# Kernel tuning notes

Hardware: AMD Instinct MI355X
Metric: run time of the kernel (lower is better)

The kernel has to match this reference:

```python
import jax, jax.numpy as jnp
import numpy as np
import math

D_MODEL = 1024
NUM_HEADS = 16
HEAD_DIM = D_MODEL // NUM_HEADS
BATCH = 2
SEQ = 2048
THETA = 10000.0


def _rope_tables(seq_len, head_dim, theta=THETA):
    inv_freq = 1.0 / theta ** (jnp.arange(0, head_dim, 2, dtype=jnp.float32) / head_dim)
    pos = jnp.arange(seq_len, dtype=jnp.float32)
    freqs = jnp.outer(pos, inv_freq)                 # [S, hd/2]
    emb = jnp.concatenate([freqs, freqs], axis=-1)   # [S, hd]
    return jnp.cos(emb), jnp.sin(emb)


def _rotate_half(x):
    x1, x2 = jnp.split(x, 2, axis=-1)
    return jnp.concatenate([-x2, x1], axis=-1)


def setup_inputs() -> dict:
    key = jax.random.key(0)
    k1, k2, k3 = jax.random.split(key, 3)
    x = jax.random.normal(k1, (BATCH, SEQ, D_MODEL), dtype=jnp.float32)
    # causal mask: 1 where attend allowed, 0 where masked
    mask = jnp.tril(jnp.ones((SEQ, SEQ), dtype=jnp.int32))[None, None]
    w_qkv = jax.random.normal(k2, (D_MODEL, 3 * D_MODEL), dtype=jnp.float32) / math.sqrt(D_MODEL)
    w_out = jax.random.normal(k3, (D_MODEL, D_MODEL), dtype=jnp.float32) / math.sqrt(D_MODEL)
    return {"x": x, "mask": mask, "w_qkv": w_qkv, "w_out": w_out}


def reference(x, mask, w_qkv, w_out):
    B, S, _ = x.shape
    qkv = x @ w_qkv                                          # [B,S,3*D]
    qkv = qkv.reshape(B, S, 3, NUM_HEADS, HEAD_DIM)
    qkv = jnp.transpose(qkv, (2, 0, 3, 1, 4))                # [3,B,H,S,hd]
    q, k, v = qkv[0], qkv[1], qkv[2]
    cos, sin = _rope_tables(S, HEAD_DIM)                     # [S,hd]
    cos = cos[None, None]; sin = sin[None, None]
    q = q * cos + _rotate_half(q) * sin
    k = k * cos + _rotate_half(k) * sin
    scores = jnp.einsum('bhqd,bhkd->bhqk', q, k) / math.sqrt(HEAD_DIM)
    scores = jnp.where(mask == 0, -jnp.inf, scores)
    attn = jax.nn.softmax(scores, axis=-1)                   # dropout p=0 (eval)
    out = jnp.einsum('bhqk,bhkd->bhqd', attn, v)             # [B,H,S,hd]
    out = jnp.transpose(out, (0, 2, 1, 3)).reshape(B, S, D_MODEL)
    return out @ w_out
```

## Files before the change

### kernel.cpp

```cpp
#include <hip/hip_runtime.h>

typedef __bf16 bf16;
typedef __bf16 bf16x4 __attribute__((ext_vector_type(4)));
typedef __bf16 bf16x8 __attribute__((ext_vector_type(8)));
typedef short s16x4 __attribute__((ext_vector_type(4)));
typedef float f32x4 __attribute__((ext_vector_type(4)));

constexpr int BATCH = 2;
constexpr int SEQ   = 2048;
constexpr int DMODEL= 1024;
constexpr int NH    = 16;
constexpr int HD    = 64;
constexpr int M_ROWS= BATCH * SEQ;
constexpr int N_QKV = 3 * DMODEL;

__device__ __forceinline__ void gl_lds16(const bf16* g, bf16* l) {
  __builtin_amdgcn_global_load_lds(
      (const __attribute__((address_space(1))) unsigned int*)g,
      (__attribute__((address_space(3))) unsigned int*)l, 16, 0, 0);
}

__device__ __forceinline__ f32x4 mfma_16x16x16_bf16(bf16x4 a, bf16x4 b,
                                                    f32x4 c) {
#if defined(__HIP_DEVICE_COMPILE__)
  union { bf16x4 h; s16x4 s; } ua{a}, ub{b};
  return __builtin_amdgcn_mfma_f32_16x16x16bf16_1k(ua.s, ub.s, c, 0, 0, 0);
#else
  return c;
#endif
}

__global__ __launch_bounds__(256) void transpose_cast_kernel(
    const float* __restrict__ src, bf16* __restrict__ dst, int R, int C) {
  __shared__ float tile[32][33];
  const int c0 = blockIdx.x * 32, r0 = blockIdx.y * 32;
  const int tx = threadIdx.x, ty = threadIdx.y;
#pragma unroll
  for (int i = 0; i < 4; i++)
    tile[ty + 8 * i][tx] = src[(size_t)(r0 + ty + 8 * i) * C + c0 + tx];
  __syncthreads();
#pragma unroll
  for (int i = 0; i < 4; i++)
    dst[(size_t)(c0 + ty + 8 * i) * R + r0 + tx] = (bf16)tile[tx][ty + 8 * i];
}

__global__ __launch_bounds__(256) void cast_f32_bf16(
    const float* __restrict__ src, bf16* __restrict__ dst) {
  const int i = (blockIdx.x * 256 + threadIdx.x) * 8;
  float4 f0 = *(const float4*)&src[i];
  float4 f1 = *(const float4*)&src[i + 4];
  bf16x8 v;
  v[0] = (bf16)f0.x; v[1] = (bf16)f0.y; v[2] = (bf16)f0.z; v[3] = (bf16)f0.w;
  v[4] = (bf16)f1.x; v[5] = (bf16)f1.y; v[6] = (bf16)f1.z; v[7] = (bf16)f1.w;
  *(bf16x8*)&dst[i] = v;
}

#define GEMM_BODY(A, BT, K)                                                    \
  __shared__ bf16 As[128 * 32];                                                \
  __shared__ bf16 Bs[128 * 32];                                                \
  const int t = threadIdx.x;                                                   \
  const int m0 = blockIdx.y * 128;                                             \
  const int n0 = blockIdx.x * 128;                                             \
  const int w = t >> 6, lane = t & 63, g = lane >> 4, li = lane & 15;          \
  const int r0w = (w & 1) * 64, c0w = (w >> 1) * 64;                           \
  f32x4 acc[4][4] = {};                                                        \
  for (int k0 = 0; k0 < (K); k0 += 32) {                                       \
    __syncthreads();                                                           \
    _Pragma("unroll") for (int c = 0; c < 2; c++) {                            \
      const int idx = (w * 2 + c) * 64 + lane;                                 \
      const int row = idx >> 2, col = (idx & 3) * 8;                           \
      gl_lds16(&(A)[(size_t)(m0 + row) * (K) + k0 + col],                      \
               &As[(w * 2 + c) * 512]);                                        \
      gl_lds16(&(BT)[(size_t)(n0 + row) * (K) + k0 + col],                     \
               &Bs[(w * 2 + c) * 512]);                                        \
    }                                                                          \
    __syncthreads();                                                           \
    bf16x8 a[4], b[4];                                                         \
    _Pragma("unroll") for (int mt = 0; mt < 4; mt++)                           \
        a[mt] = *(const bf16x8*)&As[(r0w + mt * 16 + li) * 32 + g * 8];        \
    _Pragma("unroll") for (int nt = 0; nt < 4; nt++)                           \
        b[nt] = *(const bf16x8*)&Bs[(c0w + nt * 16 + li) * 32 + g * 8];        \
    _Pragma("unroll") for (int mt = 0; mt < 4; mt++)                           \
        _Pragma("unroll") for (int nt = 0; nt < 4; nt++)                       \
            acc[mt][nt] = __builtin_amdgcn_mfma_f32_16x16x32_bf16(             \
                a[mt], b[nt], acc[mt][nt], 0, 0, 0);                           \
  }

__global__ __launch_bounds__(256) void gemm_out(
    const bf16* __restrict__ A, const bf16* __restrict__ BT,
    float* __restrict__ C, int M, int N, int K) {
  GEMM_BODY(A, BT, K)
#pragma unroll
  for (int mt = 0; mt < 4; mt++)
#pragma unroll
    for (int nt = 0; nt < 4; nt++)
#pragma unroll
      for (int r = 0; r < 4; r++) {
        const int m = m0 + r0w + mt * 16 + g * 4 + r;
        const int n = n0 + c0w + nt * 16 + li;
        C[(size_t)m * N + n] = acc[mt][nt][r];
      }
}

__global__ __launch_bounds__(256) void gemm_qkv_rope(
    const bf16* __restrict__ A, const bf16* __restrict__ BT,
    bf16* __restrict__ Qb, bf16* __restrict__ Kb, bf16* __restrict__ Vt) {
  constexpr int K = DMODEL;
  GEMM_BODY(A, BT, K)

  const int region = n0 >> 10;
  const int b = m0 >> 11;
  const int h = ((n0 + c0w) >> 6) & 15;
  const size_t bh = (size_t)(b * NH + h);

  if (region < 2) {
    bf16* dst = region == 0 ? Qb : Kb;
    const float outsc = region == 0 ? 0.125f * 1.44269504f : 1.f;
    const float L = 13.287712379549449f;
    const float if0 = exp2f(-(float)(2 * li) / 64.f * L);
    const float if1 = exp2f(-(float)(2 * (li + 16)) / 64.f * L);
#pragma unroll
    for (int mt = 0; mt < 4; mt++)
#pragma unroll
      for (int r = 0; r < 4; r++) {
        const int s = (m0 + r0w + mt * 16 + g * 4 + r) & (SEQ - 1);
        float cs[2], sn[2];
        __sincosf((float)s * if0, &sn[0], &cs[0]);
        __sincosf((float)s * if1, &sn[1], &cs[1]);
#pragma unroll
        for (int nt = 0; nt < 4; nt++) {
          const int d = nt * 16 + li;
          const int par = nt & 1;
          const float a = acc[mt][nt][r];
          const float ap = acc[mt][nt ^ 2][r];
          const float v = (nt < 2) ? a * cs[par] - ap * sn[par]
                                   : a * cs[par] + ap * sn[par];
          dst[(bh * SEQ + s) * HD + d] = (bf16)(v * outsc);
        }
      }
  } else {
#pragma unroll
    for (int mt = 0; mt < 4; mt++)
#pragma unroll
      for (int nt = 0; nt < 4; nt++) {
        const int s = (m0 + r0w + mt * 16 + g * 4) & (SEQ - 1);
        const int d = nt * 16 + li;
        bf16x4 v;
#pragma unroll
        for (int r = 0; r < 4; r++) v[r] = (bf16)acc[mt][nt][r];
        *(bf16x4*)&Vt[(bh * HD + d) * SEQ + s] = v;
      }
  }
}

__global__ __launch_bounds__(512, 4) void flash_attn6(
    const bf16* __restrict__ Q, const bf16* __restrict__ Kb,
    const bf16* __restrict__ Vt, bf16* __restrict__ Oout) {
  const int f = blockIdx.x;
  const int c = f & 255, half = f >> 8;
  const int bh = c >> 3, idx = c & 7;
  const int qt = half ? 15 - idx : idx;
  const int q0 = qt * 128;
  const int t = threadIdx.x, w = t >> 6, lane = t & 63, g = lane >> 4,
            li = lane & 15;

  __shared__ bf16 Ks[2][4096];
  __shared__ bf16 Vs[2][4096];

  const bf16* Qh = Q  + (size_t)bh * SEQ * HD;
  const bf16* Kh = Kb + (size_t)bh * SEQ * HD;
  const bf16* Vh = Vt + (size_t)bh * HD * SEQ;

  const int qw = q0 + w * 16;

  bf16x8 qf[2];
#pragma unroll
  for (int ks = 0; ks < 2; ks++)
    qf[ks] = *(const bf16x8*)&Qh[(size_t)(qw + li) * HD + ks * 32 + g * 8];

  f32x4 o[4] = {};
  float l_ = 0.f;

  const int p = w * 64 + lane;
  const int sr = p >> 3, sc = ((p & 7) ^ (sr & 7)) * 8;
  const int ldsoff = w * 512;

  const int jend = q0 + 128;
  gl_lds16(&Kh[(size_t)sr * HD + sc], &Ks[0][ldsoff]);
  gl_lds16(&Vh[(size_t)sr * SEQ + sc], &Vs[0][ldsoff]);
  __syncthreads();

  for (int j0 = 0; j0 < jend; j0 += 64) {
    const int cur = (j0 >> 6) & 1, nxt = cur ^ 1;
    if (j0 + 64 < jend) {
      const int jn = j0 + 64;
      gl_lds16(&Kh[(size_t)(jn + sr) * HD + sc], &Ks[nxt][ldsoff]);
      gl_lds16(&Vh[(size_t)sr * SEQ + jn + sc], &Vs[nxt][ldsoff]);
    }

    if (j0 <= qw + 15) {
      const bool masked = (j0 + 63 > qw);
      const int ntlim = min(4, ((qw + 15 - j0) >> 4) + 1);

      f32x4 sacc[4] = {};
#pragma unroll
      for (int ks = 0; ks < 2; ks++)
#pragma unroll
        for (int nt = 0; nt < 4; nt++) {
          if (nt >= ntlim) continue;
          const int rK = nt * 16 + li;
          const int pK = rK * 8 + ((ks * 4 + g) ^ (li & 7));
          bf16x8 kf = *(const bf16x8*)&Ks[cur][pK * 8];
          sacc[nt] = __builtin_amdgcn_mfma_f32_16x16x32_bf16(kf, qf[ks],
                                                             sacc[nt], 0, 0, 0);
        }

      bf16x4 pf[4];
#pragma unroll
      for (int nt = 0; nt < 4; nt++) {
        if (nt >= ntlim) continue;
#pragma unroll
        for (int r = 0; r < 4; r++) {
          float v = sacc[nt][r];
          if (masked) {
            const int kk = j0 + nt * 16 + g * 4 + r;
            v = (kk <= qw + li) ? v : -1e30f;
          }
          const float pe = exp2f(v);
          l_ += pe;
          pf[nt][r] = (bf16)pe;
        }
      }

#pragma unroll
      for (int nt = 0; nt < 4; nt++) {
        if (nt >= ntlim) continue;
#pragma unroll
        for (int dt = 0; dt < 4; dt++) {
          const int rV = dt * 16 + li;
          const int cg = nt * 2 + (g >> 1);
          const int pV = rV * 8 + (cg ^ (rV & 7));
          bf16x4 vfrag = *(const bf16x4*)&Vs[cur][pV * 8 + (g & 1) * 4];
          o[dt] = mfma_16x16x16_bf16(vfrag, pf[nt], o[dt]);
        }
      }
    }
    __syncthreads();
  }

  l_ += __shfl_xor(l_, 16, 64);
  l_ += __shfl_xor(l_, 32, 64);
  const float inv_l = 1.f / l_;

  const int b = bh >> 4, h = bh & 15;
  const int s = qw + li;
#pragma unroll
  for (int dt = 0; dt < 4; dt++) {
    bf16x4 ov;
#pragma unroll
    for (int r = 0; r < 4; r++) ov[r] = (bf16)(o[dt][r] * inv_l);
    *(bf16x4*)&Oout[((size_t)(b * SEQ + s)) * DMODEL + h * 64 + dt * 16 +
                    g * 4] = ov;
  }
}

extern "C" void kernel_launch(void* const* d_in, const int* in_sizes, int n_in,
                              void* d_out, int out_size, void* d_ws,
                              size_t ws_size, hipStream_t stream) {
  const float* x     = (const float*)d_in[0];
  const float* w_qkv = (const float*)d_in[2];
  const float* w_out = (const float*)d_in[3];
  float* out = (float*)d_out;

  char* ws = (char*)d_ws;
  bf16* WqkvT = (bf16*)(ws);
  bf16* WoutT = (bf16*)(ws + 6291456);
  bf16* xb    = (bf16*)(ws + 8388608);
  bf16* Qb    = (bf16*)(ws + 16777216);
  bf16* Kbuf  = (bf16*)(ws + 25165824);
  bf16* Vt    = (bf16*)(ws + 33554432);
  bf16* attn  = (bf16*)(ws + 41943040);

  cast_f32_bf16<<<M_ROWS * DMODEL / 2048, 256, 0, stream>>>(x, xb);
  transpose_cast_kernel<<<dim3(N_QKV / 32, DMODEL / 32), dim3(32, 8), 0,
                          stream>>>(w_qkv, WqkvT, DMODEL, N_QKV);
  transpose_cast_kernel<<<dim3(DMODEL / 32, DMODEL / 32), dim3(32, 8), 0,
                          stream>>>(w_out, WoutT, DMODEL, DMODEL);
  gemm_qkv_rope<<<dim3(N_QKV / 128, M_ROWS / 128), 256, 0, stream>>>(
      xb, WqkvT, Qb, Kbuf, Vt);
  flash_attn6<<<dim3(512), 512, 0, stream>>>(Qb, Kbuf, Vt, attn);
  gemm_out<<<dim3(DMODEL / 128, M_ROWS / 128), 256, 0, stream>>>(
      attn, WoutT, out, M_ROWS, DMODEL, DMODEL);
}
```

Baseline: 220.1 us.

## Quad-buffer K/V tiles with one barrier per two tiles and MFMA row sums

The flash attention kernel now keeps four K/V LDS buffers instead of two. It processes two 64-key tiles per loop iteration and issues a single __syncthreads per pair, with prefetch running two tiles ahead. The softmax denominator is now accumulated by an extra MFMA against a ones vector, replacing the per-element scalar adds and the cross-lane shuffles. This halves barrier count and moves reduction work to the matrix unit. In exchange, LDS use doubles to 64KB per block, which may cut occupancy, and the denominator now sums bf16-rounded probabilities.

```diff
diff --git a/kernel.cpp b/kernel.cpp
--- a/kernel.cpp
+++ b/kernel.cpp
@@ -153,7 +153,7 @@
   }
 }
 
-__global__ __launch_bounds__(512, 4) void flash_attn6(
+__global__ __launch_bounds__(512, 4) void flash_attn7(
     const bf16* __restrict__ Q, const bf16* __restrict__ Kb,
     const bf16* __restrict__ Vt, bf16* __restrict__ Oout) {
   const int f = blockIdx.x;
@@ -164,8 +164,8 @@
   const int t = threadIdx.x, w = t >> 6, lane = t & 63, g = lane >> 4,
             li = lane & 15;
 
-  __shared__ bf16 Ks[2][4096];
-  __shared__ bf16 Vs[2][4096];
+  __shared__ bf16 Ks[4][4096];
+  __shared__ bf16 Vs[4][4096];
 
   const bf16* Qh = Q  + (size_t)bh * SEQ * HD;
   const bf16* Kh = Kb + (size_t)bh * SEQ * HD;
@@ -179,78 +179,86 @@
     qf[ks] = *(const bf16x8*)&Qh[(size_t)(qw + li) * HD + ks * 32 + g * 8];
 
   f32x4 o[4] = {};
-  float l_ = 0.f;
+  f32x4 o4  = {};
+  bf16x4 ones;
+#pragma unroll
+  for (int r = 0; r < 4; r++) ones[r] = (bf16)1.f;
 
   const int p = w * 64 + lane;
   const int sr = p >> 3, sc = ((p & 7) ^ (sr & 7)) * 8;
   const int ldsoff = w * 512;
 
   const int jend = q0 + 128;
+
   gl_lds16(&Kh[(size_t)sr * HD + sc], &Ks[0][ldsoff]);
   gl_lds16(&Vh[(size_t)sr * SEQ + sc], &Vs[0][ldsoff]);
+  gl_lds16(&Kh[(size_t)(64 + sr) * HD + sc], &Ks[1][ldsoff]);
+  gl_lds16(&Vh[(size_t)sr * SEQ + 64 + sc], &Vs[1][ldsoff]);
   __syncthreads();
 
-  for (int j0 = 0; j0 < jend; j0 += 64) {
-    const int cur = (j0 >> 6) & 1, nxt = cur ^ 1;
-    if (j0 + 64 < jend) {
-      const int jn = j0 + 64;
-      gl_lds16(&Kh[(size_t)(jn + sr) * HD + sc], &Ks[nxt][ldsoff]);
-      gl_lds16(&Vh[(size_t)sr * SEQ + jn + sc], &Vs[nxt][ldsoff]);
+#define FA_COMPUTE(J0, BUF)                                                    \
+  if ((J0) <= qw + 15) {                                                       \
+    const bool masked = ((J0) + 63 > qw);                                      \
+    const int ntlim = min(4, ((qw + 15 - (J0)) >> 4) + 1);                     \
+    f32x4 sacc[4] = {};                                                        \
+    _Pragma("unroll") for (int ks = 0; ks < 2; ks++)                           \
+        _Pragma("unroll") for (int nt = 0; nt < 4; nt++) {                     \
+      if (nt >= ntlim) continue;                                               \
+      const int rK = nt * 16 + li;                                             \
+      const int pK = rK * 8 + ((ks * 4 + g) ^ (li & 7));                       \
+      bf16x8 kf = *(const bf16x8*)&Ks[BUF][pK * 8];                            \
+      sacc[nt] = __builtin_amdgcn_mfma_f32_16x16x32_bf16(kf, qf[ks],           \
+                                                         sacc[nt], 0, 0, 0);   \
+    }                                                                          \
+    bf16x4 pf[4];                                                              \
+    _Pragma("unroll") for (int nt = 0; nt < 4; nt++) {                         \
+      if (nt >= ntlim) continue;                                               \
+      _Pragma("unroll") for (int r = 0; r < 4; r++) {                          \
+        float v = sacc[nt][r];                                                 \
+        if (masked) {                                                          \
+          const int kk = (J0) + nt * 16 + g * 4 + r;                           \
+          v = (kk <= qw + li) ? v : -1e30f;                                    \
+        }                                                                      \
+        pf[nt][r] = (bf16)exp2f(v);                                            \
+      }                                                                        \
+    }                                                                          \
+    _Pragma("unroll") for (int nt = 0; nt < 4; nt++) {                         \
+      if (nt >= ntlim) continue;                                               \
+      o4 = mfma_16x16x16_bf16(ones, pf[nt], o4);                               \
+      _Pragma("unroll") for (int dt = 0; dt < 4; dt++) {                       \
+        const int rV = dt * 16 + li;                                           \
+        const int cg = nt * 2 + (g >> 1);                                      \
+        const int pV = rV * 8 + (cg ^ (rV & 7));                               \
+        bf16x4 vfrag = *(const bf16x4*)&Vs[BUF][pV * 8 + (g & 1) * 4];         \
+        o[dt] = mfma_16x16x16_bf16(vfrag, pf[nt], o[dt]);                      \
+      }                                                                        \
+    }                                                                          \
+  }
+
+  for (int jA = 0; jA < jend; jA += 128) {
+    const int a = (jA >> 6) & 3;
+    if (jA + 128 < jend) {
+      const int jn = jA + 128;
+      bf16* kd = &Ks[(a + 2) & 3][ldsoff];
+      bf16* vd = &Vs[(a + 2) & 3][ldsoff];
+      gl_lds16(&Kh[(size_t)(jn + sr) * HD + sc], kd);
+      gl_lds16(&Vh[(size_t)sr * SEQ + jn + sc], vd);
     }
-
-    if (j0 <= qw + 15) {
-      const bool masked = (j0 + 63 > qw);
-      const int ntlim = min(4, ((qw + 15 - j0) >> 4) + 1);
-
-      f32x4 sacc[4] = {};
-#pragma unroll
-      for (int ks = 0; ks < 2; ks++)
-#pragma unroll
-        for (int nt = 0; nt < 4; nt++) {
-          if (nt >= ntlim) continue;
-          const int rK = nt * 16 + li;
-          const int pK = rK * 8 + ((ks * 4 + g) ^ (li & 7));
-          bf16x8 kf = *(const bf16x8*)&Ks[cur][pK * 8];
-          sacc[nt] = __builtin_amdgcn_mfma_f32_16x16x32_bf16(kf, qf[ks],
-                                                             sacc[nt], 0, 0, 0);
-        }
-
-      bf16x4 pf[4];
-#pragma unroll
-      for (int nt = 0; nt < 4; nt++) {
-        if (nt >= ntlim) continue;
-#pragma unroll
-        for (int r = 0; r < 4; r++) {
-          float v = sacc[nt][r];
-          if (masked) {
-            const int kk = j0 + nt * 16 + g * 4 + r;
-            v = (kk <= qw + li) ? v : -1e30f;
-          }
-          const float pe = exp2f(v);
-          l_ += pe;
-          pf[nt][r] = (bf16)pe;
-        }
-      }
-
-#pragma unroll
-      for (int nt = 0; nt < 4; nt++) {
-        if (nt >= ntlim) continue;
-#pragma unroll
-        for (int dt = 0; dt < 4; dt++) {
-          const int rV = dt * 16 + li;
-          const int cg = nt * 2 + (g >> 1);
-          const int pV = rV * 8 + (cg ^ (rV & 7));
-          bf16x4 vfrag = *(const bf16x4*)&Vs[cur][pV * 8 + (g & 1) * 4];
-          o[dt] = mfma_16x16x16_bf16(vfrag, pf[nt], o[dt]);
-        }
-      }
+    FA_COMPUTE(jA, a)
+    const int jB = jA + 64;
+    if (jB + 128 < jend) {
+      const int jn = jB + 128;
+      bf16* kd = &Ks[(a + 3) & 3][ldsoff];
+      bf16* vd = &Vs[(a + 3) & 3][ldsoff];
+      gl_lds16(&Kh[(size_t)(jn + sr) * HD + sc], kd);
+      gl_lds16(&Vh[(size_t)sr * SEQ + jn + sc], vd);
     }
+    FA_COMPUTE(jB, ((a + 1) & 3))
     __syncthreads();
   }
-
-  l_ += __shfl_xor(l_, 16, 64);
-  l_ += __shfl_xor(l_, 32, 64);
-  const float inv_l = 1.f / l_;
+#undef FA_COMPUTE
+
+  const float inv_l = 1.f / o4[0];
 
   const int b = bh >> 4, h = bh & 15;
   const int s = qw + li;
@@ -288,7 +296,7 @@
                           stream>>>(w_out, WoutT, DMODEL, DMODEL);
   gemm_qkv_rope<<<dim3(N_QKV / 128, M_ROWS / 128), 256, 0, stream>>>(
       xb, WqkvT, Qb, Kbuf, Vt);
-  flash_attn6<<<dim3(512), 512, 0, stream>>>(Qb, Kbuf, Vt, attn);
+  flash_attn7<<<dim3(512), 512, 0, stream>>>(Qb, Kbuf, Vt, attn);
   gemm_out<<<dim3(DMODEL / 128, M_ROWS / 128), 256, 0, stream>>>(
       attn, WoutT, out, M_ROWS, DMODEL, DMODEL);
 }
```

After: 217.4 us. About the same (-1.2%).

## Shrink attention query tiles to 64 rows, compute row sums via MFMA

Applied to the files above, without the earlier changes.

The attention kernel moves from 128-query blocks of 512 threads to 64-query blocks of 256 threads. It launches 1024 blocks, scheduled in order from heaviest causal tile to lightest, in place of the paired light/heavy mapping. Each thread now issues two global-to-LDS loads per K/V tile. The softmax denominator is computed by an extra MFMA with a ones vector instead of scalar adds and cross-lane shuffles. This gives finer work granularity and better load balance, at the cost of more K/V traffic per query and one extra MFMA per tile.

```diff
diff --git a/kernel.cpp b/kernel.cpp
--- a/kernel.cpp
+++ b/kernel.cpp
@@ -153,14 +153,13 @@
   }
 }
 
-__global__ __launch_bounds__(512, 4) void flash_attn6(
+__global__ __launch_bounds__(256, 4) void flash_attn8(
     const bf16* __restrict__ Q, const bf16* __restrict__ Kb,
     const bf16* __restrict__ Vt, bf16* __restrict__ Oout) {
-  const int f = blockIdx.x;
-  const int c = f & 255, half = f >> 8;
-  const int bh = c >> 3, idx = c & 7;
-  const int qt = half ? 15 - idx : idx;
-  const int q0 = qt * 128;
+  const int bx = blockIdx.x;
+  const int qt = 31 - (bx >> 5);
+  const int bh = bx & 31;
+  const int q0 = qt * 64;
   const int t = threadIdx.x, w = t >> 6, lane = t & 63, g = lane >> 4,
             li = lane & 15;
 
@@ -179,23 +178,32 @@
     qf[ks] = *(const bf16x8*)&Qh[(size_t)(qw + li) * HD + ks * 32 + g * 8];
 
   f32x4 o[4] = {};
-  float l_ = 0.f;
-
-  const int p = w * 64 + lane;
-  const int sr = p >> 3, sc = ((p & 7) ^ (sr & 7)) * 8;
-  const int ldsoff = w * 512;
-
-  const int jend = q0 + 128;
-  gl_lds16(&Kh[(size_t)sr * HD + sc], &Ks[0][ldsoff]);
-  gl_lds16(&Vh[(size_t)sr * SEQ + sc], &Vs[0][ldsoff]);
+  f32x4 o4  = {};
+  bf16x4 ones;
+#pragma unroll
+  for (int r = 0; r < 4; r++) ones[r] = (bf16)1.f;
+
+  const int p0 = w * 128 + lane, p1 = p0 + 64;
+  const int sr0 = p0 >> 3, sc0 = ((p0 & 7) ^ (sr0 & 7)) * 8;
+  const int sr1 = p1 >> 3, sc1 = ((p1 & 7) ^ (sr1 & 7)) * 8;
+  const int lo0 = w * 1024, lo1 = w * 1024 + 512;
+
+  const int jend = q0 + 64;
+
+  gl_lds16(&Kh[(size_t)sr0 * HD + sc0], &Ks[0][lo0]);
+  gl_lds16(&Kh[(size_t)sr1 * HD + sc1], &Ks[0][lo1]);
+  gl_lds16(&Vh[(size_t)sr0 * SEQ + sc0], &Vs[0][lo0]);
+  gl_lds16(&Vh[(size_t)sr1 * SEQ + sc1], &Vs[0][lo1]);
   __syncthreads();
 
   for (int j0 = 0; j0 < jend; j0 += 64) {
     const int cur = (j0 >> 6) & 1, nxt = cur ^ 1;
     if (j0 + 64 < jend) {
       const int jn = j0 + 64;
-      gl_lds16(&Kh[(size_t)(jn + sr) * HD + sc], &Ks[nxt][ldsoff]);
-      gl_lds16(&Vh[(size_t)sr * SEQ + jn + sc], &Vs[nxt][ldsoff]);
+      gl_lds16(&Kh[(size_t)(jn + sr0) * HD + sc0], &Ks[nxt][lo0]);
+      gl_lds16(&Kh[(size_t)(jn + sr1) * HD + sc1], &Ks[nxt][lo1]);
+      gl_lds16(&Vh[(size_t)sr0 * SEQ + jn + sc0], &Vs[nxt][lo0]);
+      gl_lds16(&Vh[(size_t)sr1 * SEQ + jn + sc1], &Vs[nxt][lo1]);
     }
 
     if (j0 <= qw + 15) {
@@ -226,15 +234,14 @@
             const int kk = j0 + nt * 16 + g * 4 + r;
             v = (kk <= qw + li) ? v : -1e30f;
           }
-          const float pe = exp2f(v);
-          l_ += pe;
-          pf[nt][r] = (bf16)pe;
+          pf[nt][r] = (bf16)exp2f(v);
         }
       }
 
 #pragma unroll
       for (int nt = 0; nt < 4; nt++) {
         if (nt >= ntlim) continue;
+        o4 = mfma_16x16x16_bf16(ones, pf[nt], o4);
 #pragma unroll
         for (int dt = 0; dt < 4; dt++) {
           const int rV = dt * 16 + li;
@@ -248,9 +255,7 @@
     __syncthreads();
   }
 
-  l_ += __shfl_xor(l_, 16, 64);
-  l_ += __shfl_xor(l_, 32, 64);
-  const float inv_l = 1.f / l_;
+  const float inv_l = 1.f / o4[0];
 
   const int b = bh >> 4, h = bh & 15;
   const int s = qw + li;
@@ -288,7 +293,7 @@
                           stream>>>(w_out, WoutT, DMODEL, DMODEL);
   gemm_qkv_rope<<<dim3(N_QKV / 128, M_ROWS / 128), 256, 0, stream>>>(
       xb, WqkvT, Qb, Kbuf, Vt);
-  flash_attn6<<<dim3(512), 512, 0, stream>>>(Qb, Kbuf, Vt, attn);
+  flash_attn8<<<dim3(1024), 256, 0, stream>>>(Qb, Kbuf, Vt, attn);
   gemm_out<<<dim3(DMODEL / 128, M_ROWS / 128), 256, 0, stream>>>(
       attn, WoutT, out, M_ROWS, DMODEL, DMODEL);
 }
```

Measured after the change: 212.0 us. -3.7%, faster.
